# Kernel tuning notes

Measured on AMD Instinct MI355X. Metric: run time of the kernel, lower is better.

## Reference

```python
import jax, jax.numpy as jnp
import numpy as np

B, T, C = 8, 1024, 768
H = 12
HS = C // H  # 64


def setup_inputs() -> dict:
    key = jax.random.key(0)
    ks = jax.random.split(key, 6)
    s = C ** -0.5
    x = jax.random.normal(ks[0], (B, T, C), dtype=jnp.float32)
    Wq = jax.random.normal(ks[1], (H, C, HS), dtype=jnp.float32) * s
    Wk = jax.random.normal(ks[2], (H, C, HS), dtype=jnp.float32) * s
    Wv = jax.random.normal(ks[3], (H, C, HS), dtype=jnp.float32) * s
    Wproj = jax.random.normal(ks[4], (C, C), dtype=jnp.float32) * s
    bproj = jax.random.normal(ks[5], (C,), dtype=jnp.float32) * 0.01
    return {"x": x, "Wq": Wq, "Wk": Wk, "Wv": Wv, "Wproj": Wproj, "bproj": bproj}


def reference(x, Wq, Wk, Wv, Wproj, bproj):
    # per-head projections (equivalent to stacked per-head nn.Linear, bias=False)
    q = jnp.einsum('btc,hcd->bhtd', x, Wq)
    k = jnp.einsum('btc,hcd->bhtd', x, Wk)
    v = jnp.einsum('btc,hcd->bhtd', x, Wv)
    scale = HS ** -0.5
    scores = jnp.einsum('bhtd,bhsd->bhts', q, k) * scale  # [B,H,T,T]
    causal = jnp.tril(jnp.ones((T, T), dtype=bool))
    scores = jnp.where(causal, scores, -jnp.inf)
    weights = jax.nn.softmax(scores, axis=-1)
    out = jnp.einsum('bhts,bhsd->bhtd', weights, v)  # [B,H,T,HS]
    out = out.transpose(0, 2, 1, 3).reshape(B, T, C)  # concat heads
    # output projection (dropout is identity in eval mode)
    return out @ Wproj.T + bproj
```

## Files before the change

### kernel.cpp

```cpp
#include <hip/hip_runtime.h>
#include <hip/hip_bf16.h>


typedef short bf16x8 __attribute__((ext_vector_type(8)));
typedef float f32x4 __attribute__((ext_vector_type(4)));

static __device__ __forceinline__ unsigned short f2bf(float f) {
  unsigned int u = __float_as_uint(f);
  u += 0x7fffu + ((u >> 16) & 1u);
  return (unsigned short)(u >> 16);
}

static __device__ __forceinline__ unsigned int pk2bf(float a, float b) {
  union { __hip_bfloat162 h; unsigned int u; } c;
  c.h = __float22bfloat162_rn(make_float2(a, b));
  return c.u;
}

static __device__ __forceinline__ void gl_lds16(const void* g, void* l) {
  __builtin_amdgcn_global_load_lds(
      (const __attribute__((address_space(1))) unsigned int*)g,
      (__attribute__((address_space(3))) unsigned int*)l, 16, 0, 0);
}

#define WAIT_VM8()  asm volatile("s_waitcnt vmcnt(8)" ::: "memory")
#define WAIT_VM4()  asm volatile("s_waitcnt vmcnt(4)" ::: "memory")
#define WAIT_VM0()  asm volatile("s_waitcnt vmcnt(0)" ::: "memory")
#define BARRIER()   do { asm volatile("" ::: "memory"); \
                         __builtin_amdgcn_s_barrier();  \
                         asm volatile("" ::: "memory"); } while (0)

__global__ __launch_bounds__(256) void k_prep(
    const float* __restrict__ x, const float* __restrict__ Wproj,
    const float* __restrict__ Wq, const float* __restrict__ Wk,
    const float* __restrict__ Wv,
    unsigned short* __restrict__ xb, unsigned short* __restrict__ wp,
    unsigned short* __restrict__ wt) {
  __shared__ float tb[64][65];
  const int bx = blockIdx.x;
  const int tid = threadIdx.x;
  if (bx < 6720) {
    const float* src = (bx < 6144) ? x : Wproj;
    unsigned short* dst = (bx < 6144) ? xb : wp;
    int i = (bx < 6144 ? bx : bx - 6144) * 256 + tid;
    float4 f = ((const float4*)src)[i];
    uint2 o;
    o.x = pk2bf(f.x, f.y);
    o.y = pk2bf(f.z, f.w);
    ((uint2*)dst)[i] = o;
    return;
  }
  const int idx = bx - 6720;
  const int c0 = (idx % 12) * 64;
  const int hq = idx / 12;
  const int qi = hq / 12, h = hq % 12;
  const float* W = (qi == 0) ? Wq : ((qi == 1) ? Wk : Wv);
  {
    int rowb = tid >> 4;
    int col4 = (tid & 15) * 4;
#pragma unroll
    for (int it = 0; it < 4; ++it) {
      int c = it * 16 + rowb;
      float4 f = *(const float4*)(W + (h * 768 + c0 + c) * 64 + col4);
      tb[c][col4] = f.x; tb[c][col4 + 1] = f.y; tb[c][col4 + 2] = f.z; tb[c][col4 + 3] = f.w;
    }
  }
  __syncthreads();
#pragma unroll
  for (int it = 0; it < 2; ++it) {
    int slot = it * 256 + tid;
    int d = slot >> 3, cg = (slot & 7) * 8;
    union { unsigned int u[4]; uint4 v; } o;
#pragma unroll
    for (int j = 0; j < 4; ++j)
      o.u[j] = pk2bf(tb[cg + 2 * j][d], tb[cg + 2 * j + 1][d]);
    *(uint4*)(wt + (qi * 768 + h * 64 + d) * 768 + c0 + cg) = o.v;
  }
}

__global__ __launch_bounds__(256) void k_gemm_qkv(
    const unsigned short* __restrict__ xb,
    const unsigned short* __restrict__ wt,
    unsigned short* __restrict__ qkv,
    unsigned short* __restrict__ vt) {
  __shared__ unsigned short As0[128 * 32], As1[128 * 32];
  __shared__ unsigned short Bs0[128 * 32], Bs1[128 * 32];
  const int tid = threadIdx.x;
  const int w = tid >> 6, lane = tid & 63, quad = lane >> 4, lr = lane & 15;
  const int wm = w >> 1, wn = w & 1;
  const int m0 = blockIdx.x * 128, n0 = blockIdx.y * 128;

  f32x4 acc[4][4] = {};

  const int srow = w * 16 + (lane >> 2);
  const int su = (lane & 3) ^ ((srow >> 1) & 3);
  const int scol = su * 8;
  const unsigned short* ga0 = xb + (m0 + srow) * 768 + scol;
  const unsigned short* ga1 = ga0 + 64 * 768;
  const unsigned short* gb0 = wt + (n0 + srow) * 768 + scol;
  const unsigned short* gb1 = gb0 + 64 * 768;

  const int fu = quad ^ ((lr >> 1) & 3);

  auto stage = [&](unsigned short* lA, unsigned short* lB, int kt) {
    const int k0 = kt * 32;
    gl_lds16(ga0 + k0, lA + (w * 16) * 32);
    gl_lds16(ga1 + k0, lA + (64 + w * 16) * 32);
    gl_lds16(gb0 + k0, lB + (w * 16) * 32);
    gl_lds16(gb1 + k0, lB + (64 + w * 16) * 32);
  };
  auto compute = [&](const unsigned short* Al, const unsigned short* Bl) {
    bf16x8 af[4], bfr[4];
#pragma unroll
    for (int i = 0; i < 4; ++i)
      af[i] = *(const bf16x8*)(&Al[(wm * 64 + i * 16 + lr) * 32 + fu * 8]);
#pragma unroll
    for (int j = 0; j < 4; ++j)
      bfr[j] = *(const bf16x8*)(&Bl[(wn * 64 + j * 16 + lr) * 32 + fu * 8]);
#pragma unroll
    for (int j = 0; j < 4; ++j)
#pragma unroll
      for (int i = 0; i < 4; ++i)
        acc[j][i] = __builtin_amdgcn_mfma_f32_16x16x32_bf16(bfr[j], af[i], acc[j][i], 0, 0, 0);
  };

  stage(As0, Bs0, 0);
  stage(As1, Bs1, 1);
  for (int kt = 0; kt < 22; kt += 2) {
    WAIT_VM4();
    BARRIER();
    compute(As0, Bs0);
    BARRIER();
    stage(As0, Bs0, kt + 2);

    WAIT_VM4();
    BARRIER();
    compute(As1, Bs1);
    BARRIER();
    stage(As1, Bs1, kt + 3);
  }
  WAIT_VM4();
  BARRIER();
  compute(As0, Bs0);
  WAIT_VM0();
  BARRIER();
  compute(As1, Bs1);

  const int b = m0 >> 10, t0 = m0 & 1023;
  if (n0 < 1536) {
    const int qi = n0 / 768;
    const int rr0 = n0 - qi * 768;
#pragma unroll
    for (int j = 0; j < 4; ++j) {
      int nn = rr0 + wn * 64 + j * 16 + quad * 4;
      int h = nn >> 6, d0 = nn & 63;
      unsigned short* hb = qkv + (size_t)((qi * 8 + b) * 12 + h) * 65536 + d0;
#pragma unroll
      for (int i = 0; i < 4; ++i) {
        int t = t0 + wm * 64 + i * 16 + lr;
        uint2 o;
        o.x = pk2bf(acc[j][i][0], acc[j][i][1]);
        o.y = pk2bf(acc[j][i][2], acc[j][i][3]);
        *(uint2*)(hb + (size_t)t * 64) = o;
      }
    }
  } else {
    const int rr0 = n0 - 1536;
#pragma unroll
    for (int j = 0; j < 4; ++j) {
      int nn = rr0 + wn * 64 + j * 16 + quad * 4;
      int h = nn >> 6, d0 = nn & 63;
      unsigned short* vrow = vt + (size_t)((b * 12 + h) * 64 + d0) * 1024;
#pragma unroll
      for (int i = 0; i < 4; ++i) {
        int t = t0 + wm * 64 + i * 16 + lr;
#pragma unroll
        for (int r = 0; r < 4; ++r)
          vrow[(size_t)r * 1024 + t] = f2bf(acc[j][i][r]);
      }
    }
  }
}

__global__ __launch_bounds__(256) void k_attn(
    const unsigned short* __restrict__ qkv,
    const unsigned short* __restrict__ Vtg,
    unsigned short* __restrict__ attn) {
  __shared__ unsigned short Kbuf[2][64 * 64];
  __shared__ unsigned short Vbuf[2][64 * 64];
  __shared__ unsigned short Pbuf[4][32 * 68];
  const int tid = threadIdx.x;
  const int w = tid >> 6, lane = tid & 63, quad = lane >> 4, lr = lane & 15;
  const int hb = blockIdx.x;
  const int qb = 7 - (int)blockIdx.y;
  const int h = hb % 12, b = hb / 12;
  const int HT = 65536;
  const unsigned short* Q  = qkv + (b * 12 + h) * HT;
  const unsigned short* K  = qkv + (96 + b * 12 + h) * HT;
  const unsigned short* Vt = Vtg + (b * 12 + h) * HT;

  bf16x8 aq[2][2];
#pragma unroll
  for (int i = 0; i < 2; ++i)
#pragma unroll
    for (int hf = 0; hf < 2; ++hf)
      aq[i][hf] = *(const bf16x8*)(Q + (qb * 128 + w * 32 + i * 16 + lr) * 64 + hf * 32 + quad * 8);

  f32x4 accO[2][4] = {};
  float lsum[2] = {};

  const int nc = 2 * qb + 2;
  const float c1 = 0.125f * 1.4426950408889634f;
  const float c0 = -4.0f * 1.4426950408889634f;

  auto stage = [&](int bi, int sc) {
#pragma unroll
    for (int j = 0; j < 2; ++j) {
      int row = w * 16 + j * 8 + (lane >> 3);
      int c8 = (lane & 7) ^ (row & 7);
      gl_lds16(K + (sc * 64 + row) * 64 + c8 * 8, &Kbuf[bi][(w * 16 + j * 8) * 64]);
      gl_lds16(Vt + row * 1024 + sc * 64 + c8 * 8, &Vbuf[bi][(w * 16 + j * 8) * 64]);
    }
  };

  stage(0, 0);
  for (int sc = 0; sc < nc; ++sc) {
    __syncthreads();
    if (sc + 1 < nc) stage((sc + 1) & 1, sc + 1);
    const unsigned short* Kl = Kbuf[sc & 1];
    const unsigned short* Vl = Vbuf[sc & 1];

    f32x4 accS[2][4];
#pragma unroll
    for (int i = 0; i < 2; ++i)
#pragma unroll
      for (int nt = 0; nt < 4; ++nt) {
        f32x4 z = {};
#pragma unroll
        for (int hf = 0; hf < 2; ++hf) {
          int s = nt * 16 + lr;
          bf16x8 kb = *(const bf16x8*)(Kl + (s * 8 + ((4 * hf + quad) ^ (s & 7))) * 8);
          z = __builtin_amdgcn_mfma_f32_16x16x32_bf16(kb, aq[i][hf], z, 0, 0, 0);
        }
        accS[i][nt] = z;
      }

#pragma unroll
    for (int i = 0; i < 2; ++i) {
      const int base_i = qb * 128 + w * 32 + i * 16;
      const int tg = base_i + lr;
      const bool needmask = (sc * 64 + 63 > base_i);
      unsigned short* prow = &Pbuf[w][(i * 16 + lr) * 68];
#pragma unroll
      for (int nt = 0; nt < 4; ++nt) {
        const int sb = sc * 64 + nt * 16 + quad * 4;
        float p[4];
#pragma unroll
        for (int r = 0; r < 4; ++r) {
          float e = __builtin_amdgcn_exp2f(fmaf(accS[i][nt][r], c1, c0));
          if (needmask && (sb + r > tg)) e = 0.f;
          lsum[i] += e;
          p[r] = e;
        }
        uint2 o;
        o.x = pk2bf(p[0], p[1]);
        o.y = pk2bf(p[2], p[3]);
        *(uint2*)(prow + nt * 16 + quad * 4) = o;
      }
    }

#pragma unroll
    for (int i = 0; i < 2; ++i) {
      bf16x8 pa[2];
#pragma unroll
      for (int hf = 0; hf < 2; ++hf)
        pa[hf] = *(const bf16x8*)(&Pbuf[w][(i * 16 + lr) * 68 + hf * 32 + quad * 8]);
#pragma unroll
      for (int ntd = 0; ntd < 4; ++ntd) {
        int d = ntd * 16 + lr;
#pragma unroll
        for (int hf = 0; hf < 2; ++hf) {
          bf16x8 vb = *(const bf16x8*)(Vl + (d * 8 + ((4 * hf + quad) ^ (d & 7))) * 8);
          accO[i][ntd] = __builtin_amdgcn_mfma_f32_16x16x32_bf16(pa[hf], vb, accO[i][ntd], 0, 0, 0);
        }
      }
    }
  }

  float linv[2];
#pragma unroll
  for (int i = 0; i < 2; ++i) {
    float l = lsum[i];
    l += __shfl_xor(l, 16);
    l += __shfl_xor(l, 32);
    linv[i] = 1.0f / l;
  }
  float lri[2][4];
#pragma unroll
  for (int i = 0; i < 2; ++i)
#pragma unroll
    for (int r = 0; r < 4; ++r)
      lri[i][r] = __shfl(linv[i], quad * 4 + r);

#pragma unroll
  for (int i = 0; i < 2; ++i)
#pragma unroll
    for (int ntd = 0; ntd < 4; ++ntd) {
      int c = h * 64 + ntd * 16 + lr;
#pragma unroll
      for (int r = 0; r < 4; ++r) {
        int t = qb * 128 + w * 32 + i * 16 + quad * 4 + r;
        attn[(b * 1024 + t) * 768 + c] = f2bf(accO[i][ntd][r] * lri[i][r]);
      }
    }
}

__global__ __launch_bounds__(256) void k_gemm_proj(
    const unsigned short* __restrict__ ab,
    const unsigned short* __restrict__ wp,
    const float* __restrict__ bias,
    float* __restrict__ out) {
  __shared__ unsigned short As0[128 * 64], As1[128 * 64];
  __shared__ unsigned short Bs0[128 * 64], Bs1[128 * 64];
  const int tid = threadIdx.x;
  const int w = tid >> 6, lane = tid & 63, quad = lane >> 4, lr = lane & 15;
  const int wm = w >> 1, wn = w & 1;
  const int m0 = blockIdx.x * 128, n0 = blockIdx.y * 128;

  f32x4 acc[4][4] = {};

  const int su = (lane & 7) ^ (lane >> 3);
  const unsigned short* ga = ab + (size_t)(m0 + w * 8 + (lane >> 3)) * 768 + su * 8;
  const unsigned short* gb = wp + (size_t)(n0 + w * 8 + (lane >> 3)) * 768 + su * 8;

  auto stage = [&](unsigned short* lA, unsigned short* lB, int kt) {
    const int k0 = kt * 64;
#pragma unroll
    for (int j = 0; j < 4; ++j) {
      gl_lds16(ga + (size_t)j * 32 * 768 + k0, lA + (j * 32 + w * 8) * 64);
      gl_lds16(gb + (size_t)j * 32 * 768 + k0, lB + (j * 32 + w * 8) * 64);
    }
  };
  auto compute = [&](const unsigned short* Al, const unsigned short* Bl) {
#pragma unroll
    for (int hf = 0; hf < 2; ++hf) {
      bf16x8 af[4], bfr[4];
#pragma unroll
      for (int i = 0; i < 4; ++i)
        af[i] = *(const bf16x8*)(&Al[(wm * 64 + i * 16 + lr) * 64 + ((4 * hf + quad) ^ (lr & 7)) * 8]);
#pragma unroll
      for (int j = 0; j < 4; ++j)
        bfr[j] = *(const bf16x8*)(&Bl[(wn * 64 + j * 16 + lr) * 64 + ((4 * hf + quad) ^ (lr & 7)) * 8]);
#pragma unroll
      for (int j = 0; j < 4; ++j)
#pragma unroll
        for (int i = 0; i < 4; ++i)
          acc[j][i] = __builtin_amdgcn_mfma_f32_16x16x32_bf16(bfr[j], af[i], acc[j][i], 0, 0, 0);
    }
  };

  stage(As0, Bs0, 0);
  stage(As1, Bs1, 1);
  for (int kt = 0; kt < 10; kt += 2) {
    WAIT_VM8();
    BARRIER();
    compute(As0, Bs0);
    BARRIER();
    stage(As0, Bs0, kt + 2);

    WAIT_VM8();
    BARRIER();
    compute(As1, Bs1);
    BARRIER();
    stage(As1, Bs1, kt + 3);
  }
  WAIT_VM8();
  BARRIER();
  compute(As0, Bs0);
  WAIT_VM0();
  BARRIER();
  compute(As1, Bs1);

#pragma unroll
  for (int j = 0; j < 4; ++j) {
    int ncol = n0 + wn * 64 + j * 16 + quad * 4;
    float4 bv = *(const float4*)(bias + ncol);
#pragma unroll
    for (int i = 0; i < 4; ++i) {
      int m = m0 + wm * 64 + i * 16 + lr;
      float4 v;
      v.x = acc[j][i][0] + bv.x;
      v.y = acc[j][i][1] + bv.y;
      v.z = acc[j][i][2] + bv.z;
      v.w = acc[j][i][3] + bv.w;
      *(float4*)(out + (size_t)m * 768 + ncol) = v;
    }
  }
}

extern "C" void kernel_launch(void* const* d_in, const int* in_sizes, int n_in,
                              void* d_out, int out_size, void* d_ws, size_t ws_size,
                              hipStream_t stream) {
  const float* x     = (const float*)d_in[0];
  const float* Wq    = (const float*)d_in[1];
  const float* Wk    = (const float*)d_in[2];
  const float* Wv    = (const float*)d_in[3];
  const float* Wproj = (const float*)d_in[4];
  const float* bproj = (const float*)d_in[5];
  float* out = (float*)d_out;

  char* p = (char*)d_ws;
  unsigned short* xb   = (unsigned short*)p; p += 12582912;
  unsigned short* wt   = (unsigned short*)p; p += 3538944;
  unsigned short* wp   = (unsigned short*)p; p += 1179648;
  unsigned short* qkv  = (unsigned short*)p; p += 37748736;
  unsigned short* attn = (unsigned short*)p; p += 12582912;
  unsigned short* vt   = qkv + (size_t)192 * 65536;

  k_prep<<<7152, 256, 0, stream>>>(x, Wproj, Wq, Wk, Wv, xb, wp, wt);
  k_gemm_qkv<<<dim3(64, 18), 256, 0, stream>>>(xb, wt, qkv, vt);
  k_attn<<<dim3(96, 8), 256, 0, stream>>>(qkv, vt, attn);
  k_gemm_proj<<<dim3(64, 6), 256, 0, stream>>>(attn, wp, bproj, out);
}
```

Before: 178.2 us.

## Fuse prep, QKV GEMM, attention and projection into one cooperative persistent kernel

Replaces the four-kernel launch chain with a single cooperative kernel of 768 blocks that runs the conversion, QKV GEMM, causal attention and output projection as phases separated by grid-wide syncs. The aim is to remove launch gaps and kernel boundaries between stages. The prep phase also widens each thread's conversion to eight floats. In exchange it adds grid-sync overhead, the attention phase loses its per-block independence, and it needs 768 co-resident blocks (3 per CU). If the cooperative launch fails, it falls back to the separate kernels.

```diff
diff --git a/kernel.cpp b/kernel.cpp
--- a/kernel.cpp
+++ b/kernel.cpp
@@ -1,5 +1,8 @@
 #include <hip/hip_runtime.h>
 #include <hip/hip_bf16.h>
+#include <hip/hip_cooperative_groups.h>
+
+namespace cg = cooperative_groups;
 
 
 typedef short bf16x8 __attribute__((ext_vector_type(8)));
@@ -29,6 +32,374 @@
 #define BARRIER()   do { asm volatile("" ::: "memory"); \
                          __builtin_amdgcn_s_barrier();  \
                          asm volatile("" ::: "memory"); } while (0)
+
+union FusedSmem {
+  float tb[64][65];
+  struct { unsigned short As0[128 * 32], As1[128 * 32],
+                          Bs0[128 * 32], Bs1[128 * 32]; } g;
+  struct { unsigned short K[2][64 * 64], V[2][64 * 64],
+                          P[4][32 * 68]; } a;
+};
+
+__global__ __launch_bounds__(256, 3) void k_fused(
+    const float* __restrict__ x, const float* __restrict__ Wproj,
+    const float* __restrict__ Wq, const float* __restrict__ Wk,
+    const float* __restrict__ Wv, const float* __restrict__ bproj,
+    unsigned short* __restrict__ xb, unsigned short* __restrict__ wp,
+    unsigned short* __restrict__ wt, unsigned short* __restrict__ qkvb,
+    unsigned short* __restrict__ vt, unsigned short* __restrict__ attnb,
+    float* __restrict__ out) {
+  __shared__ FusedSmem sm;
+  cg::grid_group gridg = cg::this_grid();
+  const int tid = threadIdx.x;
+  const int bid = blockIdx.x;
+  const int w = tid >> 6, lane = tid & 63, quad = lane >> 4, lr = lane & 15;
+  const int wm = w >> 1, wn = w & 1;
+
+  for (int u = bid; u < 3792; u += 768) {
+    if (u < 3360) {
+      const float* src = (u < 3072) ? x : Wproj;
+      unsigned short* dst = (u < 3072) ? xb : wp;
+      int i = (u < 3072 ? u : u - 3072) * 256 + tid;
+      const float4* s = (const float4*)src + (size_t)i * 2;
+      float4 f0 = s[0], f1 = s[1];
+      uint4 o;
+      o.x = pk2bf(f0.x, f0.y);
+      o.y = pk2bf(f0.z, f0.w);
+      o.z = pk2bf(f1.x, f1.y);
+      o.w = pk2bf(f1.z, f1.w);
+      ((uint4*)dst)[i] = o;
+    } else {
+      const int idx = u - 3360;
+      const int c0 = (idx % 12) * 64;
+      const int hq = idx / 12;
+      const int qi = hq / 12, h = hq % 12;
+      const float* W = (qi == 0) ? Wq : ((qi == 1) ? Wk : Wv);
+      {
+        int rowb = tid >> 4;
+        int col4 = (tid & 15) * 4;
+#pragma unroll
+        for (int it = 0; it < 4; ++it) {
+          int c = it * 16 + rowb;
+          float4 f = *(const float4*)(W + (h * 768 + c0 + c) * 64 + col4);
+          sm.tb[c][col4] = f.x; sm.tb[c][col4 + 1] = f.y;
+          sm.tb[c][col4 + 2] = f.z; sm.tb[c][col4 + 3] = f.w;
+        }
+      }
+      __syncthreads();
+#pragma unroll
+      for (int it = 0; it < 2; ++it) {
+        int slot = it * 256 + tid;
+        int d = slot >> 3, cgi = (slot & 7) * 8;
+        union { unsigned int u4[4]; uint4 v; } o;
+#pragma unroll
+        for (int j = 0; j < 4; ++j)
+          o.u4[j] = pk2bf(sm.tb[cgi + 2 * j][d], sm.tb[cgi + 2 * j + 1][d]);
+        *(uint4*)(wt + (qi * 768 + h * 64 + d) * 768 + c0 + cgi) = o.v;
+      }
+      __syncthreads();
+    }
+  }
+  gridg.sync();
+
+  for (int t = bid; t < 1152; t += 768) {
+    const int m0 = (t & 63) * 128;
+    const int n0 = (t >> 6) * 128;
+    BARRIER();
+
+    f32x4 acc[4][4] = {};
+
+    const int srow = w * 16 + (lane >> 2);
+    const int su = (lane & 3) ^ ((srow >> 1) & 3);
+    const int scol = su * 8;
+    const unsigned short* ga0 = xb + (m0 + srow) * 768 + scol;
+    const unsigned short* ga1 = ga0 + 64 * 768;
+    const unsigned short* gb0 = wt + (n0 + srow) * 768 + scol;
+    const unsigned short* gb1 = gb0 + 64 * 768;
+    const int fu = quad ^ ((lr >> 1) & 3);
+
+    auto stage = [&](unsigned short* lA, unsigned short* lB, int kt) {
+      const int k0 = kt * 32;
+      gl_lds16(ga0 + k0, lA + (w * 16) * 32);
+      gl_lds16(ga1 + k0, lA + (64 + w * 16) * 32);
+      gl_lds16(gb0 + k0, lB + (w * 16) * 32);
+      gl_lds16(gb1 + k0, lB + (64 + w * 16) * 32);
+    };
+    auto compute = [&](const unsigned short* Al, const unsigned short* Bl) {
+      bf16x8 af[4], bfr[4];
+#pragma unroll
+      for (int i = 0; i < 4; ++i)
+        af[i] = *(const bf16x8*)(&Al[(wm * 64 + i * 16 + lr) * 32 + fu * 8]);
+#pragma unroll
+      for (int j = 0; j < 4; ++j)
+        bfr[j] = *(const bf16x8*)(&Bl[(wn * 64 + j * 16 + lr) * 32 + fu * 8]);
+#pragma unroll
+      for (int j = 0; j < 4; ++j)
+#pragma unroll
+        for (int i = 0; i < 4; ++i)
+          acc[j][i] = __builtin_amdgcn_mfma_f32_16x16x32_bf16(bfr[j], af[i], acc[j][i], 0, 0, 0);
+    };
+
+    stage(sm.g.As0, sm.g.Bs0, 0);
+    stage(sm.g.As1, sm.g.Bs1, 1);
+    for (int kt = 0; kt < 22; kt += 2) {
+      WAIT_VM4();
+      BARRIER();
+      compute(sm.g.As0, sm.g.Bs0);
+      BARRIER();
+      stage(sm.g.As0, sm.g.Bs0, kt + 2);
+
+      WAIT_VM4();
+      BARRIER();
+      compute(sm.g.As1, sm.g.Bs1);
+      BARRIER();
+      stage(sm.g.As1, sm.g.Bs1, kt + 3);
+    }
+    WAIT_VM4();
+    BARRIER();
+    compute(sm.g.As0, sm.g.Bs0);
+    WAIT_VM0();
+    BARRIER();
+    compute(sm.g.As1, sm.g.Bs1);
+
+    const int b = m0 >> 10, t0 = m0 & 1023;
+    if (n0 < 1536) {
+      const int qi = n0 / 768;
+      const int rr0 = n0 - qi * 768;
+#pragma unroll
+      for (int j = 0; j < 4; ++j) {
+        int nn = rr0 + wn * 64 + j * 16 + quad * 4;
+        int h = nn >> 6, d0 = nn & 63;
+        unsigned short* hb = qkvb + (size_t)((qi * 8 + b) * 12 + h) * 65536 + d0;
+#pragma unroll
+        for (int i = 0; i < 4; ++i) {
+          int tt = t0 + wm * 64 + i * 16 + lr;
+          uint2 o;
+          o.x = pk2bf(acc[j][i][0], acc[j][i][1]);
+          o.y = pk2bf(acc[j][i][2], acc[j][i][3]);
+          *(uint2*)(hb + (size_t)tt * 64) = o;
+        }
+      }
+    } else {
+      const int rr0 = n0 - 1536;
+#pragma unroll
+      for (int j = 0; j < 4; ++j) {
+        int nn = rr0 + wn * 64 + j * 16 + quad * 4;
+        int h = nn >> 6, d0 = nn & 63;
+        unsigned short* vrow = vt + (size_t)((b * 12 + h) * 64 + d0) * 1024;
+#pragma unroll
+        for (int i = 0; i < 4; ++i) {
+          int tt = t0 + wm * 64 + i * 16 + lr;
+#pragma unroll
+          for (int r = 0; r < 4; ++r)
+            vrow[(size_t)r * 1024 + tt] = f2bf(acc[j][i][r]);
+        }
+      }
+    }
+  }
+  gridg.sync();
+
+  {
+    const int hb = bid % 96;
+    const int qb = 7 - bid / 96;
+    const int h = hb % 12, b = hb / 12;
+    const int HT = 65536;
+    const unsigned short* Q  = qkvb + (b * 12 + h) * HT;
+    const unsigned short* K  = qkvb + (96 + b * 12 + h) * HT;
+    const unsigned short* Vt = vt + (b * 12 + h) * HT;
+
+    bf16x8 aq[2][2];
+#pragma unroll
+    for (int i = 0; i < 2; ++i)
+#pragma unroll
+      for (int hf = 0; hf < 2; ++hf)
+        aq[i][hf] = *(const bf16x8*)(Q + (qb * 128 + w * 32 + i * 16 + lr) * 64 + hf * 32 + quad * 8);
+
+    f32x4 accO[2][4] = {};
+    float lsum[2] = {};
+
+    const int nc = 2 * qb + 2;
+    const float c1 = 0.125f * 1.4426950408889634f;
+    const float c0 = -4.0f * 1.4426950408889634f;
+
+    auto stageA = [&](int bi, int sc) {
+#pragma unroll
+      for (int j = 0; j < 2; ++j) {
+        int row = w * 16 + j * 8 + (lane >> 3);
+        int c8 = (lane & 7) ^ (row & 7);
+        gl_lds16(K + (sc * 64 + row) * 64 + c8 * 8, &sm.a.K[bi][(w * 16 + j * 8) * 64]);
+        gl_lds16(Vt + row * 1024 + sc * 64 + c8 * 8, &sm.a.V[bi][(w * 16 + j * 8) * 64]);
+      }
+    };
+
+    stageA(0, 0);
+    for (int sc = 0; sc < nc; ++sc) {
+      __syncthreads();
+      if (sc + 1 < nc) stageA((sc + 1) & 1, sc + 1);
+      const unsigned short* Kl = sm.a.K[sc & 1];
+      const unsigned short* Vl = sm.a.V[sc & 1];
+
+      f32x4 accS[2][4];
+#pragma unroll
+      for (int i = 0; i < 2; ++i)
+#pragma unroll
+        for (int nt = 0; nt < 4; ++nt) {
+          f32x4 z = {};
+#pragma unroll
+          for (int hf = 0; hf < 2; ++hf) {
+            int s = nt * 16 + lr;
+            bf16x8 kb = *(const bf16x8*)(Kl + (s * 8 + ((4 * hf + quad) ^ (s & 7))) * 8);
+            z = __builtin_amdgcn_mfma_f32_16x16x32_bf16(kb, aq[i][hf], z, 0, 0, 0);
+          }
+          accS[i][nt] = z;
+        }
+
+#pragma unroll
+      for (int i = 0; i < 2; ++i) {
+        const int base_i = qb * 128 + w * 32 + i * 16;
+        const int tg = base_i + lr;
+        const bool needmask = (sc * 64 + 63 > base_i);
+        unsigned short* prow = &sm.a.P[w][(i * 16 + lr) * 68];
+#pragma unroll
+        for (int nt = 0; nt < 4; ++nt) {
+          const int sb = sc * 64 + nt * 16 + quad * 4;
+          float p[4];
+#pragma unroll
+          for (int r = 0; r < 4; ++r) {
+            float e = __builtin_amdgcn_exp2f(fmaf(accS[i][nt][r], c1, c0));
+            if (needmask && (sb + r > tg)) e = 0.f;
+            lsum[i] += e;
+            p[r] = e;
+          }
+          uint2 o;
+          o.x = pk2bf(p[0], p[1]);
+          o.y = pk2bf(p[2], p[3]);
+          *(uint2*)(prow + nt * 16 + quad * 4) = o;
+        }
+      }
+
+#pragma unroll
+      for (int i = 0; i < 2; ++i) {
+        bf16x8 pa[2];
+#pragma unroll
+        for (int hf = 0; hf < 2; ++hf)
+          pa[hf] = *(const bf16x8*)(&sm.a.P[w][(i * 16 + lr) * 68 + hf * 32 + quad * 8]);
+#pragma unroll
+        for (int ntd = 0; ntd < 4; ++ntd) {
+          int d = ntd * 16 + lr;
+#pragma unroll
+          for (int hf = 0; hf < 2; ++hf) {
+            bf16x8 vb = *(const bf16x8*)(Vl + (d * 8 + ((4 * hf + quad) ^ (d & 7))) * 8);
+            accO[i][ntd] = __builtin_amdgcn_mfma_f32_16x16x32_bf16(pa[hf], vb, accO[i][ntd], 0, 0, 0);
+          }
+        }
+      }
+    }
+
+    float linv[2];
+#pragma unroll
+    for (int i = 0; i < 2; ++i) {
+      float l = lsum[i];
+      l += __shfl_xor(l, 16);
+      l += __shfl_xor(l, 32);
+      linv[i] = 1.0f / l;
+    }
+    float lri[2][4];
+#pragma unroll
+    for (int i = 0; i < 2; ++i)
+#pragma unroll
+      for (int r = 0; r < 4; ++r)
+        lri[i][r] = __shfl(linv[i], quad * 4 + r);
+
+#pragma unroll
+    for (int i = 0; i < 2; ++i)
+#pragma unroll
+      for (int ntd = 0; ntd < 4; ++ntd) {
+        int c = h * 64 + ntd * 16 + lr;
+#pragma unroll
+        for (int r = 0; r < 4; ++r) {
+          int t = qb * 128 + w * 32 + i * 16 + quad * 4 + r;
+          attnb[(b * 1024 + t) * 768 + c] = f2bf(accO[i][ntd][r] * lri[i][r]);
+        }
+      }
+  }
+  gridg.sync();
+
+  if (bid < 384) {
+    const int m0 = (bid & 63) * 128, n0 = (bid >> 6) * 128;
+
+    f32x4 acc[4][4] = {};
+
+    const int srow = w * 16 + (lane >> 2);
+    const int su = (lane & 3) ^ ((srow >> 1) & 3);
+    const int scol = su * 8;
+    const unsigned short* ga0 = attnb + (m0 + srow) * 768 + scol;
+    const unsigned short* ga1 = ga0 + 64 * 768;
+    const unsigned short* gb0 = wp + (n0 + srow) * 768 + scol;
+    const unsigned short* gb1 = gb0 + 64 * 768;
+    const int fu = quad ^ ((lr >> 1) & 3);
+
+    auto stage = [&](unsigned short* lA, unsigned short* lB, int kt) {
+      const int k0 = kt * 32;
+      gl_lds16(ga0 + k0, lA + (w * 16) * 32);
+      gl_lds16(ga1 + k0, lA + (64 + w * 16) * 32);
+      gl_lds16(gb0 + k0, lB + (w * 16) * 32);
+      gl_lds16(gb1 + k0, lB + (64 + w * 16) * 32);
+    };
+    auto compute = [&](const unsigned short* Al, const unsigned short* Bl) {
+      bf16x8 af[4], bfr[4];
+#pragma unroll
+      for (int i = 0; i < 4; ++i)
+        af[i] = *(const bf16x8*)(&Al[(wm * 64 + i * 16 + lr) * 32 + fu * 8]);
+#pragma unroll
+      for (int j = 0; j < 4; ++j)
+        bfr[j] = *(const bf16x8*)(&Bl[(wn * 64 + j * 16 + lr) * 32 + fu * 8]);
+#pragma unroll
+      for (int j = 0; j < 4; ++j)
+#pragma unroll
+        for (int i = 0; i < 4; ++i)
+          acc[j][i] = __builtin_amdgcn_mfma_f32_16x16x32_bf16(bfr[j], af[i], acc[j][i], 0, 0, 0);
+    };
+
+    stage(sm.g.As0, sm.g.Bs0, 0);
+    stage(sm.g.As1, sm.g.Bs1, 1);
+    for (int kt = 0; kt < 22; kt += 2) {
+      WAIT_VM4();
+      BARRIER();
+      compute(sm.g.As0, sm.g.Bs0);
+      BARRIER();
+      stage(sm.g.As0, sm.g.Bs0, kt + 2);
+
+      WAIT_VM4();
+      BARRIER();
+      compute(sm.g.As1, sm.g.Bs1);
+      BARRIER();
+      stage(sm.g.As1, sm.g.Bs1, kt + 3);
+    }
+    WAIT_VM4();
+    BARRIER();
+    compute(sm.g.As0, sm.g.Bs0);
+    WAIT_VM0();
+    BARRIER();
+    compute(sm.g.As1, sm.g.Bs1);
+
+#pragma unroll
+    for (int j = 0; j < 4; ++j) {
+      int ncol = n0 + wn * 64 + j * 16 + quad * 4;
+      float4 bv = *(const float4*)(bproj + ncol);
+#pragma unroll
+      for (int i = 0; i < 4; ++i) {
+        int m = m0 + wm * 64 + i * 16 + lr;
+        float4 v;
+        v.x = acc[j][i][0] + bv.x;
+        v.y = acc[j][i][1] + bv.y;
+        v.z = acc[j][i][2] + bv.z;
+        v.w = acc[j][i][3] + bv.w;
+        *(float4*)(out + (size_t)m * 768 + ncol) = v;
+      }
+    }
+  }
+}
 
 __global__ __launch_bounds__(256) void k_prep(
     const float* __restrict__ x, const float* __restrict__ Wproj,
@@ -39,18 +410,21 @@
   __shared__ float tb[64][65];
   const int bx = blockIdx.x;
   const int tid = threadIdx.x;
-  if (bx < 6720) {
-    const float* src = (bx < 6144) ? x : Wproj;
-    unsigned short* dst = (bx < 6144) ? xb : wp;
-    int i = (bx < 6144 ? bx : bx - 6144) * 256 + tid;
-    float4 f = ((const float4*)src)[i];
-    uint2 o;
-    o.x = pk2bf(f.x, f.y);
-    o.y = pk2bf(f.z, f.w);
-    ((uint2*)dst)[i] = o;
+  if (bx < 3360) {
+    const float* src = (bx < 3072) ? x : Wproj;
+    unsigned short* dst = (bx < 3072) ? xb : wp;
+    int i = (bx < 3072 ? bx : bx - 3072) * 256 + tid;
+    const float4* s = (const float4*)src + (size_t)i * 2;
+    float4 f0 = s[0], f1 = s[1];
+    uint4 o;
+    o.x = pk2bf(f0.x, f0.y);
+    o.y = pk2bf(f0.z, f0.w);
+    o.z = pk2bf(f1.x, f1.y);
+    o.w = pk2bf(f1.z, f1.w);
+    ((uint4*)dst)[i] = o;
     return;
   }
-  const int idx = bx - 6720;
+  const int idx = bx - 3360;
   const int c0 = (idx % 12) * 64;
   const int hq = idx / 12;
   const int qi = hq / 12, h = hq % 12;
@@ -69,12 +443,12 @@
 #pragma unroll
   for (int it = 0; it < 2; ++it) {
     int slot = it * 256 + tid;
-    int d = slot >> 3, cg = (slot & 7) * 8;
+    int d = slot >> 3, cgi = (slot & 7) * 8;
     union { unsigned int u[4]; uint4 v; } o;
 #pragma unroll
     for (int j = 0; j < 4; ++j)
-      o.u[j] = pk2bf(tb[cg + 2 * j][d], tb[cg + 2 * j + 1][d]);
-    *(uint4*)(wt + (qi * 768 + h * 64 + d) * 768 + c0 + cg) = o.v;
+      o.u[j] = pk2bf(tb[cgi + 2 * j][d], tb[cgi + 2 * j + 1][d]);
+    *(uint4*)(wt + (qi * 768 + h * 64 + d) * 768 + c0 + cgi) = o.v;
   }
 }
 
@@ -99,7 +473,6 @@
   const unsigned short* ga1 = ga0 + 64 * 768;
   const unsigned short* gb0 = wt + (n0 + srow) * 768 + scol;
   const unsigned short* gb1 = gb0 + 64 * 768;
-
   const int fu = quad ^ ((lr >> 1) & 3);
 
   auto stage = [&](unsigned short* lA, unsigned short* lB, int kt) {
@@ -417,8 +790,16 @@
   unsigned short* attn = (unsigned short*)p; p += 12582912;
   unsigned short* vt   = qkv + (size_t)192 * 65536;
 
-  k_prep<<<7152, 256, 0, stream>>>(x, Wproj, Wq, Wk, Wv, xb, wp, wt);
-  k_gemm_qkv<<<dim3(64, 18), 256, 0, stream>>>(xb, wt, qkv, vt);
-  k_attn<<<dim3(96, 8), 256, 0, stream>>>(qkv, vt, attn);
-  k_gemm_proj<<<dim3(64, 6), 256, 0, stream>>>(attn, wp, bproj, out);
+  void* args[] = {(void*)&x, (void*)&Wproj, (void*)&Wq, (void*)&Wk, (void*)&Wv,
+                  (void*)&bproj, (void*)&xb, (void*)&wp, (void*)&wt,
+                  (void*)&qkv, (void*)&vt, (void*)&attn, (void*)&out};
+  hipError_t err = hipLaunchCooperativeKernel((const void*)k_fused, dim3(768),
+                                              dim3(256), args, 0, stream);
+  if (err != hipSuccess) {
+    (void)hipGetLastError();
+    k_prep<<<3792, 256, 0, stream>>>(x, Wproj, Wq, Wk, Wv, xb, wp, wt);
+    k_gemm_qkv<<<dim3(64, 18), 256, 0, stream>>>(xb, wt, qkv, vt);
+    k_attn<<<dim3(96, 8), 256, 0, stream>>>(qkv, vt, attn);
+    k_gemm_proj<<<dim3(64, 6), 256, 0, stream>>>(attn, wp, bproj, out);
+  }
 }
```

Result: slower. 505.4 us (+183.5%).
